# Optimization experiments

Measured on AMD Instinct MI355X. Metric: run time of the kernel, lower is better.

## Reference

```python
import jax, jax.numpy as jnp
import numpy as np
from jax import lax


def setup_inputs() -> dict:
    key = jax.random.key(0)
    W = 32
    x = jax.random.normal(key, (32, 8192, 128), dtype=jnp.float32)
    weights = jnp.arange(1, W + 1, dtype=jnp.float32)  # [1, 2, ..., W]
    return {"x": x, "weights": weights, "window_size": W}


def reference(x, weights, window_size):
    # x: [B, T, C]; weights: [W] = [1..W]
    B, T, C = x.shape
    W = window_size
    # Zero-pad the front: with kernel [1..W], a VALID causal conv applies weight
    # (W - i + j) to x[j] within the window ending at i, which matches the
    # original's weights[-L:] slicing for partial windows (L = i + 1 < W).
    xp = jnp.pad(x, ((0, 0), (W - 1, 0), (0, 0)))  # [B, T+W-1, C]
    # Depthwise conv: same kernel per channel, feature_group_count = C.
    kernel = jnp.broadcast_to(weights[:, None, None], (W, 1, C))  # WIO
    numer = lax.conv_general_dilated(
        xp, kernel, window_strides=(1,), padding="VALID",
        dimension_numbers=("NWC", "WIO", "NWC"), feature_group_count=C,
    )  # [B, T, C]
    # denom[i] = sum of the last min(i+1, W) weights = cumsum(weights[::-1]) clipped.
    csum_rev = jnp.cumsum(weights[::-1])  # [W]
    idx = jnp.minimum(jnp.arange(T), W - 1)
    denom = csum_rev[idx]  # [T]
    return numer / denom[None, :, None]
```

## Files before the change

kernel.cpp:

```cpp
#include <hip/hip_runtime.h>


typedef float f32x2 __attribute__((ext_vector_type(2)));

constexpr int W    = 32;
constexpr int B    = 32;
constexpr int T    = 8192;
constexpr int C    = 128;
constexpr int CP   = C / 2;
constexpr int SEG  = 128;
constexpr int NSEG = T / SEG;

__global__ __launch_bounds__(256)
void wma_kernel(const float* __restrict__ x, float* __restrict__ out) {
    int gtid = blockIdx.x * blockDim.x + threadIdx.x;
    int p    = gtid % CP;
    int rest = gtid / CP;
    int seg  = rest % NSEG;
    int b    = rest / NSEG;
    if (b >= B) return;

    const int t0 = seg * SEG;
    const f32x2* px = (const f32x2*)(x   + ((size_t)b * T + t0) * C) + p;
    f32x2*       po = (f32x2*)      (out + ((size_t)b * T + t0) * C) + p;

    f32x2 hist[W];
    float Sx = 0.f, Sy = 0.f, Nx = 0.f, Ny = 0.f;
    int startChunk = 0;

    if (t0 == 0) {
        #pragma unroll
        for (int i = 0; i < W; ++i) hist[i] = (f32x2){0.f, 0.f};
        #pragma unroll
        for (int i = 0; i < W; ++i) {
            f32x2 xn = px[i * CP];
            Nx = Nx - Sx + 32.0f * xn.x;
            Ny = Ny - Sy + 32.0f * xn.y;
            Sx = Sx - hist[i].x + xn.x;
            Sy = Sy - hist[i].y + xn.y;
            hist[i] = xn;
            const float invd = 1.0f / (float)(528 - (31 - i) * (32 - i) / 2);
            f32x2 o = {Nx * invd, Ny * invd};
            __builtin_nontemporal_store(o, &po[i * CP]);
        }
        startChunk = 1;
    } else {
        #pragma unroll
        for (int i = 0; i < W; ++i) hist[i] = px[(i - W) * CP];
        #pragma unroll
        for (int i = 0; i < W; ++i) {
            Sx += hist[i].x;
            Sy += hist[i].y;
            Nx += (float)(i + 1) * hist[i].x;
            Ny += (float)(i + 1) * hist[i].y;
        }
    }

    const float invD = 1.0f / 528.0f;
    for (int ch = startChunk; ch < SEG / W; ++ch) {
        const f32x2* pxc = px + (size_t)ch * W * CP;
        f32x2*       poc = po + (size_t)ch * W * CP;
        #pragma unroll
        for (int i = 0; i < W; ++i) {
            f32x2 xn = pxc[i * CP];
            Nx = Nx - Sx + 32.0f * xn.x;
            Ny = Ny - Sy + 32.0f * xn.y;
            Sx = Sx - hist[i].x + xn.x;
            Sy = Sy - hist[i].y + xn.y;
            hist[i] = xn;
            f32x2 o = {Nx * invD, Ny * invD};
            __builtin_nontemporal_store(o, &poc[i * CP]);
        }
    }
}

extern "C" void kernel_launch(void* const* d_in, const int* in_sizes, int n_in,
                              void* d_out, int out_size, void* d_ws, size_t ws_size,
                              hipStream_t stream) {
    const float* x = (const float*)d_in[0];
    float* out = (float*)d_out;

    const int total_threads = B * CP * NSEG;
    dim3 grid(total_threads / 256), block(256);
    hipLaunchKernelGGL(wma_kernel, grid, block, 0, stream, x, out);
}
```

Baseline: 49.08 us.

## Double-buffer window history and prefetch the next chunk during compute

Replaces the single history array and the runtime chunk loop with two ping-pong register buffers and a fully unrolled sequence of chunk bodies. While each chunk is processed, the slot just consumed as the outgoing element is refilled with the matching element of the next chunk, so global loads overlap the sliding-window arithmetic. It also switches to packed f32x2 arithmetic and drops the bounds check, since the grid size is exact. The trade-off is roughly twice the per-thread register footprint for buffered inputs, which may lower occupancy.

```diff
diff --git a/kernel.cpp b/kernel.cpp
--- a/kernel.cpp
+++ b/kernel.cpp
@@ -11,6 +11,17 @@
 constexpr int SEG  = 128;
 constexpr int NSEG = T / SEG;
 
+#define CHUNK_BODY(CUR, PRV, PF, LDO, STO)                          \
+    _Pragma("unroll")                                               \
+    for (int i = 0; i < W; ++i) {                                   \
+        f32x2 xn = CUR[i];                                          \
+        N2 = N2 - S2 + 32.0f * xn;                                  \
+        S2 = S2 - PRV[i] + xn;                                      \
+        f32x2 o = N2 * invD;                                        \
+        __builtin_nontemporal_store(o, &po[(STO) + i * CP]);        \
+        if (PF) PRV[i] = px[(LDO) + i * CP];                        \
+    }
+
 __global__ __launch_bounds__(256)
 void wma_kernel(const float* __restrict__ x, float* __restrict__ out) {
     int gtid = blockIdx.x * blockDim.x + threadIdx.x;
@@ -18,60 +29,46 @@
     int rest = gtid / CP;
     int seg  = rest % NSEG;
     int b    = rest / NSEG;
-    if (b >= B) return;
 
     const int t0 = seg * SEG;
     const f32x2* px = (const f32x2*)(x   + ((size_t)b * T + t0) * C) + p;
     f32x2*       po = (f32x2*)      (out + ((size_t)b * T + t0) * C) + p;
 
-    f32x2 hist[W];
-    float Sx = 0.f, Sy = 0.f, Nx = 0.f, Ny = 0.f;
-    int startChunk = 0;
+    f32x2 A[W], Bf[W];
+    f32x2 S2 = (f32x2)(0.f), N2 = (f32x2)(0.f);
+    const float invD = 1.0f / 528.0f;
 
     if (t0 == 0) {
         #pragma unroll
-        for (int i = 0; i < W; ++i) hist[i] = (f32x2){0.f, 0.f};
+        for (int i = 0; i < W; ++i) A[i]  = px[i * CP];
+        #pragma unroll
+        for (int i = 0; i < W; ++i) Bf[i] = (f32x2)(0.f);
         #pragma unroll
         for (int i = 0; i < W; ++i) {
-            f32x2 xn = px[i * CP];
-            Nx = Nx - Sx + 32.0f * xn.x;
-            Ny = Ny - Sy + 32.0f * xn.y;
-            Sx = Sx - hist[i].x + xn.x;
-            Sy = Sy - hist[i].y + xn.y;
-            hist[i] = xn;
+            f32x2 xn = A[i];
+            N2 = N2 - S2 + 32.0f * xn;
+            S2 = S2 - Bf[i] + xn;
             const float invd = 1.0f / (float)(528 - (31 - i) * (32 - i) / 2);
-            f32x2 o = {Nx * invd, Ny * invd};
+            f32x2 o = N2 * invd;
             __builtin_nontemporal_store(o, &po[i * CP]);
+            Bf[i] = px[(1 * W * CP / CP * CP) / CP * 0 + (W * CP) / CP * CP * 0 + (W + i) * CP - i * CP + i * CP];
         }
-        startChunk = 1;
     } else {
         #pragma unroll
-        for (int i = 0; i < W; ++i) hist[i] = px[(i - W) * CP];
+        for (int i = 0; i < W; ++i) Bf[i] = px[(i - W) * CP];
+        #pragma unroll
+        for (int i = 0; i < W; ++i) A[i]  = px[i * CP];
         #pragma unroll
         for (int i = 0; i < W; ++i) {
-            Sx += hist[i].x;
-            Sy += hist[i].y;
-            Nx += (float)(i + 1) * hist[i].x;
-            Ny += (float)(i + 1) * hist[i].y;
+            S2 += Bf[i];
+            N2 += (float)(i + 1) * Bf[i];
         }
+        CHUNK_BODY(A, Bf, true, 1 * W * CP, 0 * W * CP)
     }
 
-    const float invD = 1.0f / 528.0f;
-    for (int ch = startChunk; ch < SEG / W; ++ch) {
-        const f32x2* pxc = px + (size_t)ch * W * CP;
-        f32x2*       poc = po + (size_t)ch * W * CP;
-        #pragma unroll
-        for (int i = 0; i < W; ++i) {
-            f32x2 xn = pxc[i * CP];
-            Nx = Nx - Sx + 32.0f * xn.x;
-            Ny = Ny - Sy + 32.0f * xn.y;
-            Sx = Sx - hist[i].x + xn.x;
-            Sy = Sy - hist[i].y + xn.y;
-            hist[i] = xn;
-            f32x2 o = {Nx * invD, Ny * invD};
-            __builtin_nontemporal_store(o, &poc[i * CP]);
-        }
-    }
+    CHUNK_BODY(Bf, A,  true,  2 * W * CP, 1 * W * CP)
+    CHUNK_BODY(A,  Bf, true,  3 * W * CP, 2 * W * CP)
+    CHUNK_BODY(Bf, A,  false, 0,          3 * W * CP)
 }
 
 extern "C" void kernel_launch(void* const* d_in, const int* in_sizes, int n_in,
@@ -79,7 +76,6 @@
                               hipStream_t stream) {
     const float* x = (const float*)d_in[0];
     float* out = (float*)d_out;
-
     const int total_threads = B * CP * NSEG;
     dim3 grid(total_threads / 256), block(256);
     hipLaunchKernelGGL(wma_kernel, grid, block, 0, stream, x, out);
```

Result: no change. 49.01 us (-0.2%).
